# Kernel tuning notes

Hardware: AMD Instinct MI355X
Metric: run time of the kernel (lower is better)

Reference implementation:

```python
import jax, jax.numpy as jnp
import numpy as np
import math

B, T, D = 4, 4096, 1024
N, L = 256, 768
H = 16
TE = 1024  # time_embed_dim


def _ln(x, g, b, eps=1e-5):
    mu = jnp.mean(x, axis=-1, keepdims=True)
    var = jnp.var(x, axis=-1, keepdims=True)
    return (x - mu) * jax.lax.rsqrt(var + eps) * g + b


def setup_inputs() -> dict:
    key = jax.random.key(0)
    ks = jax.random.split(key, 12)
    s = lambda fan_in: 1.0 / math.sqrt(fan_in)
    return {
        "x":   jax.random.normal(ks[0], (B, T, D), jnp.float32),
        "xf":  jax.random.normal(ks[1], (B, N, L), jnp.float32),
        "emb": jax.random.normal(ks[2], (B, TE), jnp.float32),
        # LayerNorm params
        "norm_g": jnp.ones((D,), jnp.float32), "norm_b": jnp.zeros((D,), jnp.float32),
        "tnorm_g": jnp.ones((L,), jnp.float32), "tnorm_b": jnp.zeros((L,), jnp.float32),
        # Q/K/V projections
        "Wq": jax.random.uniform(ks[3], (D, D), jnp.float32, -s(D), s(D)),
        "bq": jnp.zeros((D,), jnp.float32),
        "Wk": jax.random.uniform(ks[4], (L, D), jnp.float32, -s(L), s(L)),
        "bk": jnp.zeros((D,), jnp.float32),
        "Wv": jax.random.uniform(ks[5], (L, D), jnp.float32, -s(L), s(L)),
        "bv": jnp.zeros((D,), jnp.float32),
        # StylizationBlock: emb_layers Linear(TE, 2D)
        "We": jax.random.uniform(ks[6], (TE, 2 * D), jnp.float32, -s(TE), s(TE)),
        "be": jnp.zeros((2 * D,), jnp.float32),
        # StylizationBlock: inner LayerNorm + out Linear(D, D)
        "snorm_g": jnp.ones((D,), jnp.float32), "snorm_b": jnp.zeros((D,), jnp.float32),
        "Wo": jax.random.uniform(ks[7], (D, D), jnp.float32, -s(D), s(D)),
        "bo": jnp.zeros((D,), jnp.float32),
    }


def reference(x, xf, emb, norm_g, norm_b, tnorm_g, tnorm_b,
              Wq, bq, Wk, bk, Wv, bv, We, be, snorm_g, snorm_b, Wo, bo):
    dh = D // H
    xf_n = _ln(xf, tnorm_g, tnorm_b)                      # B,N,L (shared by K and V)
    q = (_ln(x, norm_g, norm_b) @ Wq + bq).reshape(B, T, H, dh)
    k = (xf_n @ Wk + bk).reshape(B, N, H, dh)
    v = (xf_n @ Wv + bv).reshape(B, N, H, dh)
    attn = jnp.einsum('bthd,bnhd->btnh', q, k) / math.sqrt(dh)
    w = jax.nn.softmax(attn, axis=2)                      # softmax over text tokens n
    y = jnp.einsum('btnh,bnhd->bthd', w, v).reshape(B, T, D)
    # StylizationBlock (AdaLN-style)
    emb_out = jax.nn.silu(emb) @ We + be                  # B, 2D
    scale, shift = jnp.split(emb_out[:, None, :], 2, axis=2)
    h = _ln(y, snorm_g, snorm_b) * (1.0 + scale) + shift
    h = jax.nn.silu(h) @ Wo + bo
    return x + h
```

## Files before the change

kernel.cpp:

```cpp
#include <hip/hip_runtime.h>

typedef unsigned short u16;
typedef short bf16x8 __attribute__((ext_vector_type(8)));
typedef float f32x4 __attribute__((ext_vector_type(4)));


__device__ __forceinline__ float b2f(u16 u) {
  union { unsigned int u; float f; } x; x.u = ((unsigned int)u) << 16; return x.f;
}
__device__ __forceinline__ u16 f2b(float f) {
  union { float f; unsigned int u; } x; x.f = f;
  unsigned int u = x.u;
  return (u16)((u + 0x7FFFu + ((u >> 16) & 1u)) >> 16);
}

#define GLOAD_LDS16(g, l)                                                      \
  __builtin_amdgcn_global_load_lds(                                            \
      (const __attribute__((address_space(1))) unsigned int*)(g),              \
      (__attribute__((address_space(3))) unsigned int*)(l), 16, 0, 0)

__global__ __launch_bounds__(256) void transpose4_k(
    const float* __restrict__ Wq, const float* __restrict__ Wk,
    const float* __restrict__ Wv, const float* __restrict__ Wo,
    u16* __restrict__ wqt, u16* __restrict__ wkt,
    u16* __restrict__ wvt, u16* __restrict__ wot,
    float* __restrict__ embo) {
  if (blockIdx.z == 0 && blockIdx.y == 0) {
    int idx = blockIdx.x * 256 + threadIdx.y * 32 + threadIdx.x;
    embo[idx] = 0.f;
  }
  const float* src; u16* dst; int R;
  switch (blockIdx.z) {
    case 0: src = Wq; dst = wqt; R = 1024; break;
    case 1: src = Wk; dst = wkt; R = 768;  break;
    case 2: src = Wv; dst = wvt; R = 768;  break;
    default: src = Wo; dst = wot; R = 1024; break;
  }
  int bx = blockIdx.x * 32, by = blockIdx.y * 32;
  if (by >= R) return;
  __shared__ float t[32][33];
  int x = threadIdx.x, y = threadIdx.y;
#pragma unroll
  for (int i = 0; i < 4; ++i)
    t[y * 4 + i][x] = src[(size_t)(by + y * 4 + i) * 1024 + bx + x];
  __syncthreads();
#pragma unroll
  for (int i = 0; i < 4; ++i)
    dst[(size_t)(bx + y * 4 + i) * R + by + x] = f2b(t[x][y * 4 + i]);
}

__global__ __launch_bounds__(256) void ln_k(const float* __restrict__ in,
                                            const float* __restrict__ g,
                                            const float* __restrict__ bta,
                                            u16* __restrict__ out, int C) {
  int row = blockIdx.x, tid = threadIdx.x;
  const float* p = in + (size_t)row * C;
  int i0 = tid * 4;
  bool act = i0 < C;
  float v0 = 0.f, v1 = 0.f, v2 = 0.f, v3 = 0.f;
  if (act) {
    float4 u = *(const float4*)(p + i0);
    v0 = u.x; v1 = u.y; v2 = u.z; v3 = u.w;
  }
  float s = v0 + v1 + v2 + v3;
  float q = v0 * v0 + v1 * v1 + v2 * v2 + v3 * v3;
  __shared__ float red[8];
#pragma unroll
  for (int m = 32; m; m >>= 1) { s += __shfl_xor(s, m); q += __shfl_xor(q, m); }
  if ((tid & 63) == 0) { red[tid >> 6] = s; red[4 + (tid >> 6)] = q; }
  __syncthreads();
  s = red[0] + red[1] + red[2] + red[3];
  q = red[4] + red[5] + red[6] + red[7];
  float invC = 1.0f / (float)C;
  float mu = s * invC;
  float rs = rsqrtf(q * invC - mu * mu + 1e-5f);
  if (act) {
    float4 ug = *(const float4*)(g + i0);
    float4 ub = *(const float4*)(bta + i0);
    ushort4 o;
    o.x = f2b((v0 - mu) * rs * ug.x + ub.x);
    o.y = f2b((v1 - mu) * rs * ug.y + ub.y);
    o.z = f2b((v2 - mu) * rs * ug.z + ub.z);
    o.w = f2b((v3 - mu) * rs * ug.w + ub.w);
    *(ushort4*)(out + (size_t)row * C + i0) = o;
  }
}

__global__ __launch_bounds__(256) void style_k(const u16* __restrict__ y,
                                               const float* __restrict__ g,
                                               const float* __restrict__ bta,
                                               const float* __restrict__ embo,
                                               u16* __restrict__ out) {
  int row = blockIdx.x, tid = threadIdx.x;
  int b = row >> 12;
  const u16* p = y + (size_t)row * 1024;
  int i0 = tid * 4;
  ushort4 u = *(const ushort4*)(p + i0);
  float v0 = b2f(u.x), v1 = b2f(u.y), v2 = b2f(u.z), v3 = b2f(u.w);
  float s = v0 + v1 + v2 + v3;
  float q = v0 * v0 + v1 * v1 + v2 * v2 + v3 * v3;
  __shared__ float red[8];
#pragma unroll
  for (int m = 32; m; m >>= 1) { s += __shfl_xor(s, m); q += __shfl_xor(q, m); }
  if ((tid & 63) == 0) { red[tid >> 6] = s; red[4 + (tid >> 6)] = q; }
  __syncthreads();
  s = red[0] + red[1] + red[2] + red[3];
  q = red[4] + red[5] + red[6] + red[7];
  const float invC = 1.0f / 1024.0f;
  float mu = s * invC;
  float rs = rsqrtf(q * invC - mu * mu + 1e-5f);
  float4 ug = *(const float4*)(g + i0);
  float4 ub = *(const float4*)(bta + i0);
  float4 sc = *(const float4*)(embo + b * 2048 + i0);
  float4 sh = *(const float4*)(embo + b * 2048 + 1024 + i0);
  float h0 = ((v0 - mu) * rs * ug.x + ub.x) * (1.0f + sc.x) + sh.x;
  float h1 = ((v1 - mu) * rs * ug.y + ub.y) * (1.0f + sc.y) + sh.y;
  float h2 = ((v2 - mu) * rs * ug.z + ub.z) * (1.0f + sc.z) + sh.z;
  float h3 = ((v3 - mu) * rs * ug.w + ub.w) * (1.0f + sc.w) + sh.w;
  ushort4 o;
  o.x = f2b(h0 / (1.0f + __expf(-h0)));
  o.y = f2b(h1 / (1.0f + __expf(-h1)));
  o.z = f2b(h2 / (1.0f + __expf(-h2)));
  o.w = f2b(h3 / (1.0f + __expf(-h3)));
  *(ushort4*)(out + (size_t)row * 1024 + i0) = o;
}

__global__ __launch_bounds__(256) void emb_k(const float* __restrict__ emb,
                                             const float* __restrict__ We,
                                             const float* __restrict__ be,
                                             float* __restrict__ embo) {
  int b = blockIdx.y, tid = threadIdx.x;
  int j = blockIdx.x * 256 + tid;
  int i0 = blockIdx.z * 128;
  __shared__ float se[128];
  if (tid < 128) {
    float v = emb[b * 1024 + i0 + tid];
    se[tid] = v / (1.0f + __expf(-v));
  }
  __syncthreads();
  float acc = (blockIdx.z == 0) ? be[j] : 0.f;
#pragma unroll 8
  for (int i = 0; i < 128; ++i) acc += se[i] * We[(size_t)(i0 + i) * 2048 + j];
  atomicAdd(&embo[b * 2048 + j], acc);
}

__global__ __launch_bounds__(256) void gemm_bt_k(const u16* __restrict__ A,
                                                 const u16* __restrict__ Bt,
                                                 const float* __restrict__ bias,
                                                 const float* __restrict__ res,
                                                 u16* __restrict__ Cb,
                                                 float* __restrict__ Cf,
                                                 int M, int Nn, int K, int mode) {
  __shared__ __align__(16) short As[128 * 64];
  __shared__ __align__(16) short Bs[128 * 64];
  int tid = threadIdx.x;
  int m0 = blockIdx.x * 128, n0 = blockIdx.y * 128;
  int wave = tid >> 6, lane = tid & 63;
  int l16 = lane & 15, quad = lane >> 4;
  int wm = (wave >> 1) * 64, wn = (wave & 1) * 64;

  f32x4 acc[4][4];
#pragma unroll
  for (int i = 0; i < 4; ++i)
#pragma unroll
    for (int j = 0; j < 4; ++j)
#pragma unroll
      for (int r = 0; r < 4; ++r) acc[i][j][r] = 0.f;

  for (int kt = 0; kt < K; kt += 64) {
#pragma unroll
    for (int p = 0; p < 4; ++p) {
      int c = p * 256 + tid;
      int r = c >> 3;
      int cd = ((c & 7) ^ (r & 7)) * 8;
      int lb = (p * 256 + wave * 64) * 8;
      GLOAD_LDS16(A + (size_t)(m0 + r) * K + kt + cd, As + lb);
      GLOAD_LDS16(Bt + (size_t)(n0 + r) * K + kt + cd, Bs + lb);
    }
    __syncthreads();
#pragma unroll
    for (int ks = 0; ks < 2; ++ks) {
      int swz = ((ks * 4 + quad) ^ (l16 & 7)) * 8;
      bf16x8 af[4], bfr[4];
#pragma unroll
      for (int i = 0; i < 4; ++i)
        af[i] = *(const bf16x8*)&As[(wm + i * 16 + l16) * 64 + swz];
#pragma unroll
      for (int j = 0; j < 4; ++j)
        bfr[j] = *(const bf16x8*)&Bs[(wn + j * 16 + l16) * 64 + swz];
#pragma unroll
      for (int i = 0; i < 4; ++i)
#pragma unroll
        for (int j = 0; j < 4; ++j)
          acc[i][j] = __builtin_amdgcn_mfma_f32_16x16x32_bf16(af[i], bfr[j], acc[i][j], 0, 0, 0);
    }
    __syncthreads();
  }

#pragma unroll
  for (int j = 0; j < 4; ++j) {
    int col = n0 + wn + j * 16 + l16;
    float bv = bias[col];
#pragma unroll
    for (int i = 0; i < 4; ++i) {
      int row0 = m0 + wm + i * 16 + quad * 4;
#pragma unroll
      for (int r = 0; r < 4; ++r) {
        int row = row0 + r;
        float v = acc[i][j][r] + bv;
        if (mode == 2) {
          Cf[(size_t)row * Nn + col] = v + res[(size_t)row * Nn + col];
        } else if (mode == 1) {
          Cb[((size_t)((row >> 8) * 1024 + col)) * 256 + (row & 255)] = f2b(v);
        } else {
          Cb[(size_t)row * Nn + col] = f2b(v);
        }
      }
    }
  }
}

__global__ __launch_bounds__(512, 2) void gemm256_k(const u16* __restrict__ A,
                                                    const u16* __restrict__ Bt,
                                                    const float* __restrict__ bias,
                                                    const float* __restrict__ res,
                                                    u16* __restrict__ Cb,
                                                    float* __restrict__ Cf,
                                                    int M, int Nn, int K, int mode) {
  __shared__ __align__(16) short smem[2][4][256 * 32];
  int tid = threadIdx.x;
  int m0 = blockIdx.x * 256, n0 = blockIdx.y * 256;
  int wave = tid >> 6, lane = tid & 63;
  int l16 = lane & 15, quad = lane >> 4;
  int wm = (wave >> 2) * 128;
  int wn = (wave & 3) * 64;

  size_t offA[2], offB[2];
  int ldsOff[2];
#pragma unroll
  for (int p = 0; p < 2; ++p) {
    int c = p * 512 + tid;
    int r = c >> 2;
    int cg = (c & 3) ^ ((r >> 1) & 3);
    offA[p] = (size_t)(m0 + r) * K + cg * 8;
    offB[p] = (size_t)(n0 + r) * K + cg * 8;
    ldsOff[p] = (p * 512 + wave * 64) * 8;
  }

  int aoff[8], boff[4];
#pragma unroll
  for (int mi = 0; mi < 8; ++mi) {
    int R = wm + mi * 16 + l16;
    aoff[mi] = R * 32 + ((quad ^ ((R >> 1) & 3)) * 8);
  }
#pragma unroll
  for (int ni = 0; ni < 4; ++ni) {
    int R = wn + ni * 16 + l16;
    boff[ni] = R * 32 + ((quad ^ ((R >> 1) & 3)) * 8);
  }

  f32x4 acc[8][4];
#pragma unroll
  for (int i = 0; i < 8; ++i)
#pragma unroll
    for (int j = 0; j < 4; ++j)
#pragma unroll
      for (int r = 0; r < 4; ++r) acc[i][j][r] = 0.f;

#define STAGE(tt, bufc)                                                        \
  do {                                                                         \
    int kt_ = (tt) * 32;                                                       \
    GLOAD_LDS16(A + offA[0] + kt_, &smem[0][bufc][0] + ldsOff[0]);             \
    GLOAD_LDS16(A + offA[1] + kt_, &smem[0][bufc][0] + ldsOff[1]);             \
    GLOAD_LDS16(Bt + offB[0] + kt_, &smem[1][bufc][0] + ldsOff[0]);            \
    GLOAD_LDS16(Bt + offB[1] + kt_, &smem[1][bufc][0] + ldsOff[1]);            \
  } while (0)

#define TILE(tc, bufc, WAITN, DOSTAGE)                                         \
  do {                                                                         \
    asm volatile("s_waitcnt vmcnt(" #WAITN ")" ::: "memory");                  \
    __builtin_amdgcn_s_barrier();                                              \
    asm volatile("" ::: "memory");                                             \
    if (DOSTAGE) STAGE((tc) + 3, ((bufc) + 3) & 3);                            \
    bf16x8 af[8], bfv[4];                                                      \
    _Pragma("unroll") for (int mi = 0; mi < 8; ++mi)                           \
        af[mi] = *(const bf16x8*)&smem[0][bufc][aoff[mi]];                     \
    _Pragma("unroll") for (int ni = 0; ni < 4; ++ni)                           \
        bfv[ni] = *(const bf16x8*)&smem[1][bufc][boff[ni]];                    \
    __builtin_amdgcn_s_setprio(1);                                             \
    _Pragma("unroll") for (int mi = 0; mi < 8; ++mi)                           \
      _Pragma("unroll") for (int ni = 0; ni < 4; ++ni)                         \
        acc[mi][ni] = __builtin_amdgcn_mfma_f32_16x16x32_bf16(                 \
            af[mi], bfv[ni], acc[mi][ni], 0, 0, 0);                            \
    __builtin_amdgcn_s_setprio(0);                                             \
  } while (0)

  const int NT = K >> 5;
  STAGE(0, 0);
  STAGE(1, 1);
  STAGE(2, 2);

  int t4 = 0;
  for (; t4 + 8 <= NT; t4 += 4) {
    TILE(t4 + 0, 0, 8, 1);
    TILE(t4 + 1, 1, 8, 1);
    TILE(t4 + 2, 2, 8, 1);
    TILE(t4 + 3, 3, 8, 1);
  }
  TILE(t4 + 0, 0, 8, 1);
  TILE(t4 + 1, 1, 8, 0);
  TILE(t4 + 2, 2, 4, 0);
  TILE(t4 + 3, 3, 0, 0);
#undef TILE
#undef STAGE

  float* eps = (float*)&smem[0][0][0];
  float bv[4];
#pragma unroll
  for (int ni = 0; ni < 4; ++ni) bv[ni] = bias[n0 + wn + ni * 16 + l16];

#pragma unroll
  for (int half = 0; half < 2; ++half) {
    __syncthreads();
    if ((wave >> 2) == half) {
#pragma unroll
      for (int mi = 0; mi < 8; ++mi) {
#pragma unroll
        for (int ni = 0; ni < 4; ++ni) {
          int col = wn + ni * 16 + l16;
#pragma unroll
          for (int r = 0; r < 4; ++r) {
            int row = mi * 16 + quad * 4 + r;
            eps[row * 256 + (col ^ (((row >> 2) & 3) << 3))] =
                acc[mi][ni][r] + bv[ni];
          }
        }
      }
    }
    __syncthreads();
#pragma unroll
    for (int p = 0; p < 16; ++p) {
      int row = wave * 16 + p;
      int grow = m0 + half * 128 + row;
      int colb = (lane * 4) ^ (((row >> 2) & 3) << 3);
      f32x4 v = *(const f32x4*)&eps[row * 256 + colb];
      if (mode == 2) {
        float4 rv = ((const float4*)&res[(size_t)grow * Nn + n0])[lane];
        float4 o;
        o.x = v[0] + rv.x; o.y = v[1] + rv.y;
        o.z = v[2] + rv.z; o.w = v[3] + rv.w;
        ((float4*)&Cf[(size_t)grow * Nn + n0])[lane] = o;
      } else {
        ushort4 o;
        o.x = f2b(v[0]); o.y = f2b(v[1]); o.z = f2b(v[2]); o.w = f2b(v[3]);
        ((ushort4*)&Cb[(size_t)grow * Nn + n0])[lane] = o;
      }
    }
  }
}

__global__ __launch_bounds__(256) void attn_k(const u16* __restrict__ Q,
                                              const u16* __restrict__ Kt,
                                              const u16* __restrict__ VT,
                                              u16* __restrict__ Y) {
  __shared__ __align__(16) short KsPs[256 * 64];
  __shared__ __align__(16) short Vt[64 * 256];
  int tid = threadIdx.x;
  int t0 = blockIdx.x * 64, h = blockIdx.y, b = blockIdx.z;
  int wave = tid >> 6, lane = tid & 63;
  int l16 = lane & 15, quad = lane >> 4;
  int wb = wave * 16;

#pragma unroll
  for (int p = 0; p < 8; ++p) {
    int c = tid + p * 256;
    int n = c >> 3, cd = c & 7;
    *(int4*)&KsPs[n * 64 + ((cd ^ (n & 7)) * 8)] =
        *(const int4*)(Kt + ((size_t)(b * 256 + n)) * 1024 + h * 64 + cd * 8);
  }
#pragma unroll
  for (int p = 0; p < 8; ++p) {
    int c = tid + p * 256;
    int d = c >> 5, ch = c & 31;
    *(int4*)&Vt[d * 256 + ((ch ^ (d & 7)) * 8)] =
        *(const int4*)(VT + ((size_t)(b * 1024 + h * 64 + d)) * 256 + ch * 8);
  }
  const u16* qrow = Q + ((size_t)(b * 4096 + t0 + wb + l16)) * 1024 + h * 64;
  bf16x8 qf0 = *(const bf16x8*)(qrow + quad * 8);
  bf16x8 qf1 = *(const bf16x8*)(qrow + 32 + quad * 8);
  __syncthreads();

  f32x4 sa[16];
#pragma unroll
  for (int nt = 0; nt < 16; ++nt)
#pragma unroll
    for (int r = 0; r < 4; ++r) sa[nt][r] = 0.f;
#pragma unroll
  for (int ks = 0; ks < 2; ++ks) {
    bf16x8 af = ks ? qf1 : qf0;
#pragma unroll
    for (int nt = 0; nt < 16; ++nt) {
      int n = nt * 16 + l16;
      bf16x8 bfr = *(const bf16x8*)&KsPs[n * 64 + (((ks * 4 + quad) ^ (n & 7)) * 8)];
      sa[nt] = __builtin_amdgcn_mfma_f32_16x16x32_bf16(af, bfr, sa[nt], 0, 0, 0);
    }
  }
  __syncthreads();

#pragma unroll
  for (int r = 0; r < 4; ++r) {
    float mx = -3.0e38f;
#pragma unroll
    for (int nt = 0; nt < 16; ++nt) mx = fmaxf(mx, sa[nt][r]);
    mx = fmaxf(mx, __shfl_xor(mx, 1));
    mx = fmaxf(mx, __shfl_xor(mx, 2));
    mx = fmaxf(mx, __shfl_xor(mx, 4));
    mx = fmaxf(mx, __shfl_xor(mx, 8));
    float e[16];
    float sum = 0.f;
#pragma unroll
    for (int nt = 0; nt < 16; ++nt) {
      e[nt] = __expf((sa[nt][r] - mx) * 0.125f);
      sum += e[nt];
    }
    sum += __shfl_xor(sum, 1);
    sum += __shfl_xor(sum, 2);
    sum += __shfl_xor(sum, 4);
    sum += __shfl_xor(sum, 8);
    float rsc = 1.0f / sum;
    int prow = wb + quad * 4 + r;
#pragma unroll
    for (int nt = 0; nt < 16; ++nt) {
      int col = nt * 16 + l16;
      KsPs[prow * 256 + (((col >> 3) ^ (prow & 7)) * 8) + (col & 7)] =
          (short)f2b(e[nt] * rsc);
    }
  }
  __syncthreads();

  f32x4 ya[4];
#pragma unroll
  for (int j = 0; j < 4; ++j)
#pragma unroll
    for (int r = 0; r < 4; ++r) ya[j][r] = 0.f;
  int m = wb + l16;
#pragma unroll
  for (int kk = 0; kk < 8; ++kk) {
    bf16x8 af = *(const bf16x8*)&KsPs[m * 256 + (((kk * 4 + quad) ^ (m & 7)) * 8)];
#pragma unroll
    for (int j = 0; j < 4; ++j) {
      int d = j * 16 + l16;
      bf16x8 bfr = *(const bf16x8*)&Vt[d * 256 + (((kk * 4 + quad) ^ (d & 7)) * 8)];
      ya[j] = __builtin_amdgcn_mfma_f32_16x16x32_bf16(af, bfr, ya[j], 0, 0, 0);
    }
  }
#pragma unroll
  for (int j = 0; j < 4; ++j)
#pragma unroll
    for (int r = 0; r < 4; ++r)
      Y[((size_t)(b * 4096 + t0 + wb + quad * 4 + r)) * 1024 + h * 64 + j * 16 + l16] =
          f2b(ya[j][r]);
}

extern "C" void kernel_launch(void* const* d_in, const int* in_sizes, int n_in,
                              void* d_out, int out_size, void* d_ws, size_t ws_size,
                              hipStream_t stream) {
  const float* x       = (const float*)d_in[0];
  const float* xf      = (const float*)d_in[1];
  const float* emb     = (const float*)d_in[2];
  const float* norm_g  = (const float*)d_in[3];
  const float* norm_b  = (const float*)d_in[4];
  const float* tnorm_g = (const float*)d_in[5];
  const float* tnorm_b = (const float*)d_in[6];
  const float* Wq      = (const float*)d_in[7];
  const float* bq      = (const float*)d_in[8];
  const float* Wk      = (const float*)d_in[9];
  const float* bk      = (const float*)d_in[10];
  const float* Wv      = (const float*)d_in[11];
  const float* bv      = (const float*)d_in[12];
  const float* We      = (const float*)d_in[13];
  const float* be      = (const float*)d_in[14];
  const float* snorm_g = (const float*)d_in[15];
  const float* snorm_b = (const float*)d_in[16];
  const float* Wo      = (const float*)d_in[17];
  const float* bo      = (const float*)d_in[18];

  const size_t MB = 1024 * 1024;
  char* dout = (char*)d_out;
  u16* qbuf = (u16*)(dout);
  u16* wqt  = (u16*)(dout + 32 * MB);
  u16* wkt  = (u16*)(dout + 34 * MB);
  u16* wvt  = (u16*)(dout + 36 * MB);
  float* out = (float*)d_out;

  char* ws = (char*)d_ws;
  u16* big1 = (u16*)(ws);
  u16* xfn  = (u16*)(ws + 32 * MB);
  u16* kws  = (u16*)(ws + 33 * MB + 512 * 1024);
  u16* vtws = (u16*)(ws + 35 * MB + 512 * 1024);
  u16* wot  = (u16*)(ws + 37 * MB + 512 * 1024);
  float* embo = (float*)(ws + 39 * MB + 512 * 1024);

  transpose4_k<<<dim3(32, 32, 4), dim3(32, 8), 0, stream>>>(
      Wq, Wk, Wv, Wo, wqt, wkt, wvt, wot, embo);

  ln_k<<<16384, 256, 0, stream>>>(x, norm_g, norm_b, big1, 1024);
  ln_k<<<1024, 256, 0, stream>>>(xf, tnorm_g, tnorm_b, xfn, 768);

  gemm256_k<<<dim3(64, 4), 512, 0, stream>>>(big1, wqt, bq, nullptr, qbuf, nullptr, 16384, 1024, 1024, 0);
  gemm_bt_k<<<dim3(8, 8), 256, 0, stream>>>(xfn, wkt, bk, nullptr, kws, nullptr, 1024, 1024, 768, 0);
  gemm_bt_k<<<dim3(8, 8), 256, 0, stream>>>(xfn, wvt, bv, nullptr, vtws, nullptr, 1024, 1024, 768, 1);

  emb_k<<<dim3(8, 4, 8), 256, 0, stream>>>(emb, We, be, embo);

  attn_k<<<dim3(64, 16, 4), 256, 0, stream>>>(qbuf, kws, vtws, big1);

  style_k<<<16384, 256, 0, stream>>>(big1, snorm_g, snorm_b, embo, big1);

  gemm256_k<<<dim3(64, 4), 512, 0, stream>>>(big1, wot, bo, x, nullptr, out, 16384, 1024, 1024, 2);
}
```

Before: 378.4 us.

## Compute transposed scores so softmax reduces in-lane and defers normalization

The QK^T MFMA now swaps its operands, so each lane holds one query's scores across key tiles. The softmax max and sum become mostly in-register reductions with two cross-lane shuffles instead of four per row. Exponentials use exp2 with a prefolded log2e/sqrt(dh) constant, and P is packed to bf16 with v_cvt_pk_bf16_f32 and written to LDS as 8-byte stores. The 1/sum normalization moves to the output, applied after the PV MFMA through a shuffle, which removes per-element multiplies before the bf16 rounding.

```diff
diff --git a/kernel.cpp b/kernel.cpp
--- a/kernel.cpp
+++ b/kernel.cpp
@@ -392,48 +392,55 @@
 
   f32x4 sa[16];
 #pragma unroll
-  for (int nt = 0; nt < 16; ++nt)
-#pragma unroll
-    for (int r = 0; r < 4; ++r) sa[nt][r] = 0.f;
+  for (int mt = 0; mt < 16; ++mt)
+#pragma unroll
+    for (int r = 0; r < 4; ++r) sa[mt][r] = 0.f;
 #pragma unroll
   for (int ks = 0; ks < 2; ++ks) {
-    bf16x8 af = ks ? qf1 : qf0;
-#pragma unroll
-    for (int nt = 0; nt < 16; ++nt) {
-      int n = nt * 16 + l16;
-      bf16x8 bfr = *(const bf16x8*)&KsPs[n * 64 + (((ks * 4 + quad) ^ (n & 7)) * 8)];
-      sa[nt] = __builtin_amdgcn_mfma_f32_16x16x32_bf16(af, bfr, sa[nt], 0, 0, 0);
-    }
-  }
-  __syncthreads();
-
-#pragma unroll
-  for (int r = 0; r < 4; ++r) {
-    float mx = -3.0e38f;
-#pragma unroll
-    for (int nt = 0; nt < 16; ++nt) mx = fmaxf(mx, sa[nt][r]);
-    mx = fmaxf(mx, __shfl_xor(mx, 1));
-    mx = fmaxf(mx, __shfl_xor(mx, 2));
-    mx = fmaxf(mx, __shfl_xor(mx, 4));
-    mx = fmaxf(mx, __shfl_xor(mx, 8));
-    float e[16];
-    float sum = 0.f;
-#pragma unroll
-    for (int nt = 0; nt < 16; ++nt) {
-      e[nt] = __expf((sa[nt][r] - mx) * 0.125f);
-      sum += e[nt];
-    }
-    sum += __shfl_xor(sum, 1);
-    sum += __shfl_xor(sum, 2);
-    sum += __shfl_xor(sum, 4);
-    sum += __shfl_xor(sum, 8);
-    float rsc = 1.0f / sum;
-    int prow = wb + quad * 4 + r;
-#pragma unroll
-    for (int nt = 0; nt < 16; ++nt) {
-      int col = nt * 16 + l16;
-      KsPs[prow * 256 + (((col >> 3) ^ (prow & 7)) * 8) + (col & 7)] =
-          (short)f2b(e[nt] * rsc);
+    bf16x8 qb = ks ? qf1 : qf0;
+#pragma unroll
+    for (int mt = 0; mt < 16; ++mt) {
+      int n = mt * 16 + l16;
+      bf16x8 kf = *(const bf16x8*)&KsPs[n * 64 + (((ks * 4 + quad) ^ (n & 7)) * 8)];
+      sa[mt] = __builtin_amdgcn_mfma_f32_16x16x32_bf16(kf, qb, sa[mt], 0, 0, 0);
+    }
+  }
+  __syncthreads();
+
+  const float CLG = 0.18033688011112042f;
+  float mx = -3.0e38f;
+#pragma unroll
+  for (int mt = 0; mt < 16; ++mt)
+#pragma unroll
+    for (int r = 0; r < 4; ++r) mx = fmaxf(mx, sa[mt][r]);
+  mx = fmaxf(mx, __shfl_xor(mx, 16));
+  mx = fmaxf(mx, __shfl_xor(mx, 32));
+  float mxc = mx * CLG;
+  float sum = 0.f;
+#pragma unroll
+  for (int mt = 0; mt < 16; ++mt)
+#pragma unroll
+    for (int r = 0; r < 4; ++r) {
+      float e = __builtin_exp2f(sa[mt][r] * CLG - mxc);
+      sa[mt][r] = e;
+      sum += e;
+    }
+  sum += __shfl_xor(sum, 16);
+  sum += __shfl_xor(sum, 32);
+  float rsc = 1.0f / sum;
+
+  {
+    int prow = wb + l16;
+    short* pb = &KsPs[prow * 256 + (quad & 1) * 4];
+    int q2 = quad >> 1, swz = l16 & 7;
+#pragma unroll
+    for (int mt = 0; mt < 16; ++mt) {
+      float a0 = sa[mt][0], a1 = sa[mt][1], a2 = sa[mt][2], a3 = sa[mt][3];
+      unsigned plo, phi;
+      asm("v_cvt_pk_bf16_f32 %0, %1, %2" : "=v"(plo) : "v"(a0), "v"(a1));
+      asm("v_cvt_pk_bf16_f32 %0, %1, %2" : "=v"(phi) : "v"(a2), "v"(a3));
+      uint2 pk; pk.x = plo; pk.y = phi;
+      *(uint2*)(pb + (((2 * mt + q2) ^ swz) * 8)) = pk;
     }
   }
   __syncthreads();
@@ -454,12 +461,15 @@
       ya[j] = __builtin_amdgcn_mfma_f32_16x16x32_bf16(af, bfr, ya[j], 0, 0, 0);
     }
   }
+  float rscv[4];
+#pragma unroll
+  for (int r = 0; r < 4; ++r) rscv[r] = __shfl(rsc, quad * 4 + r);
 #pragma unroll
   for (int j = 0; j < 4; ++j)
 #pragma unroll
     for (int r = 0; r < 4; ++r)
       Y[((size_t)(b * 4096 + t0 + wb + quad * 4 + r)) * 1024 + h * 64 + j * 16 + l16] =
-          f2b(ya[j][r]);
+          f2b(ya[j][r] * rscv[r]);
 }
 
 extern "C" void kernel_launch(void* const* d_in, const int* in_sizes, int n_in,
```

Measured after the change: 376.7 us. Within noise of the previous version (-0.5%).
